# Optimization experiments

Hardware: AMD Instinct MI355X
Metric: run time of the kernel (lower is better)

Reference implementation:

```python
import jax, jax.numpy as jnp
import numpy as np

R = 16       # voxel resolution
CH = 64      # channels
NSAMPLE = 16
PROJ = 3


def _bn(x, p, eps):
    # p: [4, C] rows = (gamma, beta, running_mean, running_var); eval-mode BN
    g, b, m, v = p
    sh = [1] * x.ndim
    sh[1] = -1
    return (x - m.reshape(sh)) * (g.reshape(sh) * jax.lax.rsqrt(v.reshape(sh) + eps)) + b.reshape(sh)


def _gather_ch(x, flat_idx):
    # x: [B, C, M], flat_idx: [B, L] -> [B, C, L]
    B, C, _ = x.shape
    idx = jnp.broadcast_to(flat_idx[:, None, :], (B, C, flat_idx.shape[1]))
    return jnp.take_along_axis(x, idx, axis=2)


def _pvb_forward(x, xyz, idx, w3d1, b3d1, bn3d1, w3d2, b3d2, bn3d2, proj_w1, proj_bn, proj_w2, pt_bn):
    B, C, N = x.shape
    r = R
    # ---------- voxelization (coords detached, normalize=False) ----------
    nc = xyz - xyz.mean(axis=2, keepdims=True)
    nc = jnp.clip((nc + 1.0) * 0.5 * r, 0.0, r - 1.0)
    nc = jax.lax.stop_gradient(nc)                        # [B,3,N] float in [0, r-1]
    vi = jnp.round(nc).astype(jnp.int32)
    flat = (vi[:, 0] * r + vi[:, 1]) * r + vi[:, 2]       # [B,N]
    seg = (flat + jnp.arange(B, dtype=jnp.int32)[:, None] * (r ** 3)).reshape(-1)
    feats = x.transpose(0, 2, 1).reshape(B * N, C)
    sums = jax.ops.segment_sum(feats, seg, num_segments=B * r ** 3)
    cnts = jax.ops.segment_sum(jnp.ones((B * N,), x.dtype), seg, num_segments=B * r ** 3)
    v = (sums / jnp.maximum(cnts, 1.0)[:, None]).reshape(B, r, r, r, C).transpose(0, 4, 1, 2, 3)
    # ---------- depthwise Conv3d -> BN3d -> LeakyReLU (x2) ----------
    dn = ('NCDHW', 'OIDHW', 'NCDHW')
    v = jax.lax.conv_general_dilated(v, w3d1, (1, 1, 1), 'SAME', dimension_numbers=dn,
                                     feature_group_count=C) + b3d1.reshape(1, C, 1, 1, 1)
    v = jax.nn.leaky_relu(_bn(v, bn3d1, 1e-4), 0.1)
    v = jax.lax.conv_general_dilated(v, w3d2, (1, 1, 1), 'SAME', dimension_numbers=dn,
                                     feature_group_count=C) + b3d2.reshape(1, C, 1, 1, 1)
    v = jax.nn.leaky_relu(_bn(v, bn3d2, 1e-4), 0.1)
    # ---------- trilinear devoxelize ----------
    vf = v.reshape(B, C, r ** 3)
    lo = jnp.floor(nc).astype(jnp.int32)
    fr = nc - lo
    hi = jnp.minimum(lo + 1, r - 1)
    p_v_x = jnp.zeros((B, C, N), x.dtype)
    for dx in (0, 1):
        for dy in (0, 1):
            for dz in (0, 1):
                xi = hi[:, 0] if dx else lo[:, 0]
                yi = hi[:, 1] if dy else lo[:, 1]
                zi = hi[:, 2] if dz else lo[:, 2]
                w = ((fr[:, 0] if dx else 1.0 - fr[:, 0]) *
                     (fr[:, 1] if dy else 1.0 - fr[:, 1]) *
                     (fr[:, 2] if dz else 1.0 - fr[:, 2]))
                p_v_x = p_v_x + w[:, None, :] * _gather_ch(vf, (xi * r + yi) * r + zi)
    # ---------- neighbor gather (precomputed ball-query idx) ----------
    K = idx.shape[-1]
    flat_nb = idx.reshape(B, N * K)
    x_j = _gather_ch(x, flat_nb).reshape(B, C, N, K)
    xyz_j = _gather_ch(xyz, flat_nb).reshape(B, 3, N, K)
    dp1 = xyz_j - xyz[:, :, :, None]                      # [B,3,N,K]
    df = x_j - x[:, :, :, None]                           # [B,C,N,K]
    # proj_conv: 1x1 conv -> BN2d -> ReLU -> 1x1 conv
    h = jnp.einsum('oc,bcnk->bonk', proj_w1, df)
    h = jax.nn.relu(_bn(h, proj_bn, 1e-5))
    dp2 = jnp.einsum('oc,bcnk->bonk', proj_w2, h)         # [B,3,N,K]
    dp = jnp.concatenate([dp1, dp2], axis=1)              # [B,6,N,K]
    # repeat_interleave of the 6 channels up to C (last gets remainder)
    part = 6
    rep = C // part
    repeats = np.array([rep] * (part - 1) + [C - rep * (part - 1)])
    w = jnp.repeat(dp, repeats, axis=1, total_repeat_length=C)
    x_j = x_j * w
    x_j = jax.nn.relu(_bn(x_j, pt_bn, 1e-5))              # proj_transform
    p_p_x = x_j.max(axis=-1)                              # max-pool over neighbors
    return p_v_x + p_p_x                                  # agg_way == 'add'


def setup_inputs() -> dict:
    key = jax.random.key(0)
    ks = jax.random.split(key, 16)
    B, C, N, K = 4, CH, 16384, NSAMPLE

    def bn_params(k, c):
        k1, k2, k3, k4 = jax.random.split(k, 4)
        return jnp.stack([1.0 + 0.1 * jax.random.normal(k1, (c,), jnp.float32),
                          0.1 * jax.random.normal(k2, (c,), jnp.float32),
                          0.1 * jax.random.normal(k3, (c,), jnp.float32),
                          jax.random.uniform(k4, (c,), jnp.float32, 0.5, 1.5)])

    return dict(
        x=jax.random.normal(ks[0], (B, C, N), jnp.float32),
        xyz=jax.random.uniform(ks[1], (B, 3, N), jnp.float32, -1.0, 1.0),
        idx=jax.random.randint(ks[2], (B, N, K), 0, N, jnp.int32),
        w3d1=0.1 * jax.random.normal(ks[3], (C, 1, 3, 3, 3), jnp.float32),
        b3d1=0.01 * jax.random.normal(ks[4], (C,), jnp.float32),
        bn3d1=bn_params(ks[5], C),
        w3d2=0.1 * jax.random.normal(ks[6], (C, 1, 3, 3, 3), jnp.float32),
        b3d2=0.01 * jax.random.normal(ks[7], (C,), jnp.float32),
        bn3d2=bn_params(ks[8], C),
        proj_w1=0.1 * jax.random.normal(ks[9], (PROJ, C), jnp.float32),
        proj_bn=bn_params(ks[10], PROJ),
        proj_w2=0.3 * jax.random.normal(ks[11], (PROJ, PROJ), jnp.float32),
        pt_bn=bn_params(ks[12], C),
    )


def reference(x, xyz, idx, w3d1, b3d1, bn3d1, w3d2, b3d2, bn3d2, proj_w1, proj_bn, proj_w2, pt_bn):
    return _pvb_forward(x, xyz, idx, w3d1, b3d1, bn3d1, w3d2, b3d2, bn3d2, proj_w1, proj_bn, proj_w2, pt_bn)
```

## Files before the change

kernel.cpp:

```cpp
#include <hip/hip_runtime.h>

namespace {
constexpr int B_  = 4;
constexpr int C_  = 64;
constexpr int N_  = 16384;
constexpr int K_  = 16;
constexpr int R3_ = 4096;

constexpr int OFF_MEANS = 0;
constexpr int OFF_XT    = 16;
constexpr int OFF_PTS   = OFF_XT   + B_*N_*C_/2;
constexpr int OFF_PTSH  = OFF_PTS  + B_*N_*8;
constexpr int OFF_SUMS  = OFF_PTSH + B_*N_*4;
constexpr int OFF_CNTS  = OFF_SUMS + B_*R3_*C_;
constexpr int OFF_VT16  = OFF_CNTS + B_*R3_;
constexpr int OFF_VOX2  = OFF_VT16 + B_*C_*R3_/2;
constexpr int FILL_FLOATS = B_*R3_*C_ + B_*R3_;
constexpr int FILL_BLOCKS = FILL_FLOATS / (256 * 4);
}

__device__ __forceinline__ unsigned short f2bf(float f) {
  unsigned u = __float_as_uint(f);
  return (unsigned short)((u + 0x7FFFu + ((u >> 16) & 1u)) >> 16);
}
__device__ __forceinline__ unsigned cvtpk_bf16(float lo, float hi) {
  unsigned r;
  asm("v_cvt_pk_bf16_f32 %0, %1, %2" : "=v"(r) : "v"(lo), "v"(hi));
  return r;
}
__device__ __forceinline__ float bflo(unsigned u) { return __uint_as_float(u << 16); }
__device__ __forceinline__ float bfhi(unsigned u) { return __uint_as_float(u & 0xffff0000u); }

__global__ __launch_bounds__(256) void k_init(
    const float* __restrict__ xyz, float* __restrict__ means,
    float* __restrict__ fill) {
  const int blk = blockIdx.x;
  if (blk >= 12) {
    const int base = (blk - 12) * (256 * 4) + threadIdx.x * 4;
    *(float4*)(fill + base) = make_float4(0.f, 0.f, 0.f, 0.f);
    return;
  }
  __shared__ double red[256];
  const float* p = xyz + blk * N_;
  double s = 0.0;
  for (int i = threadIdx.x; i < N_; i += 256) s += (double)p[i];
  red[threadIdx.x] = s;
  __syncthreads();
  for (int st = 128; st; st >>= 1) {
    if (threadIdx.x < st) red[threadIdx.x] += red[threadIdx.x + st];
    __syncthreads();
  }
  if (threadIdx.x == 0) means[blk] = (float)(red[0] * (1.0 / (double)N_));
}

__global__ __launch_bounds__(256) void k_prep(
    const float* __restrict__ x, const float* __restrict__ xyz,
    const float* __restrict__ pw1, const float* __restrict__ means,
    unsigned short* __restrict__ xT, float* __restrict__ pts,
    unsigned* __restrict__ ptsh,
    float* __restrict__ sums, float* __restrict__ cnts) {
  __shared__ float tile[64 * 65];
  __shared__ float ncs[3][64];
  __shared__ float xys[3][64];
  __shared__ float hps[3][64];
  __shared__ int   flats[64];

  const int t   = threadIdx.x;
  const int blk = blockIdx.x;
  const int b   = blk >> 8;
  const int n0  = (blk & 255) << 6;

#pragma unroll
  for (int i = 0; i < 4; ++i) {
    int c = i * 16 + (t >> 4);
    int j4 = (t & 15) * 4;
    float4 v = *(const float4*)&x[((size_t)(b * C_ + c)) * N_ + n0 + j4];
    tile[c * 65 + j4 + 0] = v.x;
    tile[c * 65 + j4 + 1] = v.y;
    tile[c * 65 + j4 + 2] = v.z;
    tile[c * 65 + j4 + 3] = v.w;
  }
  __syncthreads();

  unsigned* __restrict__ xT32 = (unsigned*)xT;
#pragma unroll
  for (int i = 0; i < 8; ++i) {
    int p = i * 8 + (t >> 5);
    int c2 = (t & 31) * 2;
    unsigned pk = cvtpk_bf16(tile[c2 * 65 + p], tile[(c2 + 1) * 65 + p]);
    xT32[((size_t)(b * N_ + n0 + p)) * 32 + (t & 31)] = pk;
  }

  if (t < 192) {
    int p = t & 63, q = t >> 6;
    float s = 0.f;
#pragma unroll
    for (int c = 0; c < 64; ++c) s = fmaf(pw1[q * 64 + c], tile[c * 65 + p], s);
    size_t pb = ((size_t)(b * N_ + n0 + p)) * 8;
    pts[pb + 3 + q] = s;
    hps[q][p] = s;
    float v = xyz[((size_t)(b * 3 + q)) * N_ + n0 + p];
    pts[pb + q] = v;
    xys[q][p] = v;
    float nc = fminf(fmaxf((v - means[b * 3 + q] + 1.0f) * 8.0f, 0.0f), 15.0f);
    ncs[q][p] = nc;
  } else {
    int p = t & 63;
    size_t pb = ((size_t)(b * N_ + n0 + p)) * 8;
    pts[pb + 6] = 0.f;
    pts[pb + 7] = 0.f;
  }
  __syncthreads();

  if (t < 64) {
    int vx = (int)rintf(ncs[0][t]);
    int vy = (int)rintf(ncs[1][t]);
    int vz = (int)rintf(ncs[2][t]);
    int f = (vx * 16 + vy) * 16 + vz;
    flats[t] = f;
    atomicAdd(&cnts[b * R3_ + f], 1.0f);
    uint4 r;
    r.x = cvtpk_bf16(xys[0][t], xys[1][t]);
    r.y = cvtpk_bf16(xys[2][t], hps[0][t]);
    r.z = cvtpk_bf16(hps[1][t], hps[2][t]);
    r.w = 0u;
    *(uint4*)&ptsh[((size_t)(b * N_ + n0 + t)) * 4] = r;
  }
  __syncthreads();

  const int w = t >> 6, lane = t & 63;
#pragma unroll
  for (int i = 0; i < 16; ++i) {
    int p = w * 16 + i;
    int f = flats[p];
    atomicAdd(&sums[((size_t)(b * R3_ + f)) * C_ + lane], tile[lane * 65 + p]);
  }
}

__global__ __launch_bounds__(256) void k_tr(
    const float* __restrict__ sums, const float* __restrict__ cnts,
    unsigned* __restrict__ vT16) {
  __shared__ float tile[64 * 65];
  __shared__ float rs[64];
  const int t = threadIdx.x;
  const int b = blockIdx.x >> 6;
  const int v0 = (blockIdx.x & 63) << 6;

#pragma unroll
  for (int i = 0; i < 16; ++i) {
    int r = i * 4 + (t >> 6);
    int c = t & 63;
    tile[r * 65 + c] = sums[((size_t)(b * R3_ + v0 + r)) * C_ + c];
  }
  if (t < 64) rs[t] = 1.0f / fmaxf(cnts[b * R3_ + v0 + t], 1.0f);
  __syncthreads();

#pragma unroll
  for (int i = 0; i < 8; ++i) {
    int d = t + i * 256;
    int c = d >> 5, vp = (d & 31) * 2;
    unsigned pk = cvtpk_bf16(tile[vp * 65 + c] * rs[vp],
                             tile[(vp + 1) * 65 + c] * rs[vp + 1]);
    vT16[((size_t)(b * C_ + c)) * 2048 + (v0 >> 1) + (d & 31)] = pk;
  }
}

__global__ __launch_bounds__(256) void k_conv(
    const unsigned* __restrict__ vT16,
    const float* __restrict__ w3d1, const float* __restrict__ b3d1,
    const float* __restrict__ bn1, const float* __restrict__ w3d2,
    const float* __restrict__ b3d2, const float* __restrict__ bn2,
    unsigned short* __restrict__ vox2) {
  __shared__ float va[18 * 18 * 20];
  __shared__ float vb[18 * 18 * 20];
  const int t = threadIdx.x;
  const int b = blockIdx.x >> 6;
  const int c = blockIdx.x & 63;

  float W1[27], W2[27];
#pragma unroll
  for (int i = 0; i < 27; ++i) { W1[i] = w3d1[c * 27 + i]; W2[i] = w3d2[c * 27 + i]; }
  const float s1 = bn1[c] / sqrtf(bn1[192 + c] + 1e-4f);
  const float d1 = (b3d1[c] - bn1[128 + c]) * s1 + bn1[64 + c];
  const float s2 = bn2[c] / sqrtf(bn2[192 + c] + 1e-4f);
  const float d2 = (b3d2[c] - bn2[128 + c]) * s2 + bn2[64 + c];

  for (int i = t; i < 18 * 18 * 20; i += 256) { va[i] = 0.f; vb[i] = 0.f; }
  const unsigned* __restrict__ vrow = vT16 + ((size_t)(b * C_ + c)) * 2048;
  __syncthreads();

#pragma unroll
  for (int i = 0; i < 8; ++i) {
    int d = t + i * 256;
    unsigned u = vrow[d];
    int vox0 = d * 2;
    int z = vox0 & 15, y = (vox0 >> 4) & 15, xx = vox0 >> 8;
    int base = ((xx + 1) * 18 + (y + 1)) * 20 + (z + 1);
    va[base]     = bflo(u);
    va[base + 1] = bfhi(u);
  }
  __syncthreads();

  const int x = t >> 4, y = t & 15;
  float acc[16];

#pragma unroll
  for (int z = 0; z < 16; ++z) acc[z] = 0.f;
#pragma unroll
  for (int dx = 0; dx < 3; ++dx)
#pragma unroll
    for (int dy = 0; dy < 3; ++dy) {
      const float* row = &va[((x + dx) * 18 + (y + dy)) * 20];
      float wv[18];
      *(float4*)&wv[0]  = *(const float4*)&row[0];
      *(float4*)&wv[4]  = *(const float4*)&row[4];
      *(float4*)&wv[8]  = *(const float4*)&row[8];
      *(float4*)&wv[12] = *(const float4*)&row[12];
      wv[16] = row[16]; wv[17] = row[17];
      const float k0 = W1[(dx * 3 + dy) * 3 + 0];
      const float k1 = W1[(dx * 3 + dy) * 3 + 1];
      const float k2 = W1[(dx * 3 + dy) * 3 + 2];
#pragma unroll
      for (int z = 0; z < 16; ++z)
        acc[z] = fmaf(k0, wv[z], fmaf(k1, wv[z + 1], fmaf(k2, wv[z + 2], acc[z])));
    }
  {
    const int wb = ((x + 1) * 18 + (y + 1)) * 20 + 1;
#pragma unroll
    for (int z = 0; z < 16; ++z) {
      float tt = acc[z] * s1 + d1;
      vb[wb + z] = tt > 0.f ? tt : 0.1f * tt;
    }
  }
  __syncthreads();

#pragma unroll
  for (int z = 0; z < 16; ++z) acc[z] = 0.f;
#pragma unroll
  for (int dx = 0; dx < 3; ++dx)
#pragma unroll
    for (int dy = 0; dy < 3; ++dy) {
      const float* row = &vb[((x + dx) * 18 + (y + dy)) * 20];
      float wv[18];
      *(float4*)&wv[0]  = *(const float4*)&row[0];
      *(float4*)&wv[4]  = *(const float4*)&row[4];
      *(float4*)&wv[8]  = *(const float4*)&row[8];
      *(float4*)&wv[12] = *(const float4*)&row[12];
      wv[16] = row[16]; wv[17] = row[17];
      const float k0 = W2[(dx * 3 + dy) * 3 + 0];
      const float k1 = W2[(dx * 3 + dy) * 3 + 1];
      const float k2 = W2[(dx * 3 + dy) * 3 + 2];
#pragma unroll
      for (int z = 0; z < 16; ++z)
        acc[z] = fmaf(k0, wv[z], fmaf(k1, wv[z + 1], fmaf(k2, wv[z + 2], acc[z])));
    }
  {
    const int vbase = (x * 16 + y) * 16;
#pragma unroll
    for (int z = 0; z < 16; ++z) {
      float tt = acc[z] * s2 + d2;
      vox2[((size_t)(b * R3_ + vbase + z)) * C_ + c] = f2bf(tt > 0.f ? tt : 0.1f * tt);
    }
  }
}

__global__ __launch_bounds__(256, 8) void k_final(
    const unsigned short* __restrict__ xT, const float* __restrict__ pts,
    const unsigned* __restrict__ ptsh,
    const unsigned short* __restrict__ vox2, const int* __restrict__ idx,
    const float* __restrict__ means, const float* __restrict__ pbn,
    const float* __restrict__ pw2, const float* __restrict__ ptbn,
    float* __restrict__ out) {
  __shared__ unsigned w6[3][513];
  __shared__ int      jarr[512];
  __shared__ unsigned dv[32][8];
  __shared__ float    outT[64 * 33];

  const int t = threadIdx.x;
  const int blk = blockIdx.x;
  const int xcd = blk & 7;
  const int b = xcd >> 1;
  const int t32 = ((blk >> 3) << 1) | (xcd & 1);
  const int n0 = t32 * 32;

  const float psc0 = pbn[0] * rsqrtf(pbn[9]  + 1e-5f);
  const float psc1 = pbn[1] * rsqrtf(pbn[10] + 1e-5f);
  const float psc2 = pbn[2] * rsqrtf(pbn[11] + 1e-5f);
  const float pof0 = pbn[3] - pbn[6] * psc0;
  const float pof1 = pbn[4] - pbn[7] * psc1;
  const float pof2 = pbn[5] - pbn[8] * psc2;
  float W2r[9];
#pragma unroll
  for (int i = 0; i < 9; ++i) W2r[i] = pw2[i];

  const float* __restrict__ ptsb = pts + (size_t)b * N_ * 8;
  const unsigned* __restrict__ ptshb = ptsh + (size_t)b * N_ * 4;

#pragma unroll
  for (int rep = 0; rep < 2; ++rep) {
    const int q = t + rep * 256;
    const int p = q >> 4;
    const int n = n0 + p;
    const int j = idx[(size_t)b * N_ * K_ + (size_t)n0 * K_ + q];
    jarr[q] = j;
    uint4 q4 = *(const uint4*)(ptshb + (size_t)j * 4);
    const float qx0 = bflo(q4.x), qx1 = bfhi(q4.x);
    const float qx2 = bflo(q4.y), qh0 = bfhi(q4.y);
    const float qh1 = bflo(q4.z), qh2 = bfhi(q4.z);
    const float* ir = ptsb + (size_t)n * 8;
    float4 pa = *(const float4*)ir;
    float4 pb = *(const float4*)(ir + 4);
    float d0 = qx0 - pa.x, d1 = qx1 - pa.y, d2 = qx2 - pa.z;
    float c0 = pof0 - psc0 * pa.w;
    float c1 = pof1 - psc1 * pb.x;
    float c2 = pof2 - psc2 * pb.y;
    float h0 = fmaxf(fmaf(qh0, psc0, c0), 0.f);
    float h1 = fmaxf(fmaf(qh1, psc1, c1), 0.f);
    float h2 = fmaxf(fmaf(qh2, psc2, c2), 0.f);
    float e0 = fmaf(W2r[0], h0, fmaf(W2r[1], h1, W2r[2] * h2));
    float e1 = fmaf(W2r[3], h0, fmaf(W2r[4], h1, W2r[5] * h2));
    float e2 = fmaf(W2r[6], h0, fmaf(W2r[7], h1, W2r[8] * h2));
    w6[0][q] = cvtpk_bf16(d0, d1);
    w6[1][q] = cvtpk_bf16(d2, e0);
    w6[2][q] = cvtpk_bf16(e1, e2);
  }

  if (t < 32) {
    const int n = n0 + t;
    const float* ir = ptsb + (size_t)n * 8;
    float x0 = ir[0], x1 = ir[1], x2 = ir[2];
    float nc0 = fminf(fmaxf((x0 - means[b * 3 + 0] + 1.0f) * 8.0f, 0.0f), 15.0f);
    float nc1 = fminf(fmaxf((x1 - means[b * 3 + 1] + 1.0f) * 8.0f, 0.0f), 15.0f);
    float nc2 = fminf(fmaxf((x2 - means[b * 3 + 2] + 1.0f) * 8.0f, 0.0f), 15.0f);
    int lx = (int)nc0, ly = (int)nc1, lz = (int)nc2;
    float fx = nc0 - (float)lx, fy = nc1 - (float)ly, fz = nc2 - (float)lz;
    int hx = lx < 15 ? lx + 1 : 15;
    int hy = ly < 15 ? ly + 1 : 15;
    int hz = lz < 15 ? lz + 1 : 15;
    float wx[2] = {1.f - fx, fx};
    float wy[2] = {1.f - fy, fy};
    float wz[2] = {1.f - fz, fz};
    int xi[2] = {lx, hx}, yi[2] = {ly, hy}, zi[2] = {lz, hz};
#pragma unroll
    for (int c8 = 0; c8 < 8; ++c8) {
      int dx = c8 >> 2, dy = (c8 >> 1) & 1, dz = c8 & 1;
      int flat = (xi[dx] * 16 + yi[dy]) * 16 + zi[dz];
      float wt = wx[dx] * wy[dy] * wz[dz];
      dv[t][c8] = ((unsigned)flat << 16) | (unsigned)f2bf(wt);
    }
  }
  __syncthreads();

  const int w = t >> 6, lane = t & 63;
  const unsigned voff = (unsigned)lane * 2u;
  const int widx = lane < 20 ? 0 : lane < 40 ? 1 : 2;
  const bool hi = (lane >= 10 && lane < 20) || (lane >= 30 && lane < 40) || (lane >= 50);
  const unsigned shl = hi ? 0u : 16u;
  const float ts = ptbn[lane] * rsqrtf(ptbn[192 + lane] + 1e-5f);
  const float td = ptbn[64 + lane] - ptbn[128 + lane] * ts;
  const unsigned short* __restrict__ xTb = xT + (size_t)b * N_ * C_;
  const unsigned short* __restrict__ voxb = vox2 + (size_t)b * R3_ * C_;

  float g[24];
#pragma unroll
  for (int z = 0; z < 24; ++z) g[z] = 0.f;

#pragma unroll
  for (int i = 0; i < 8; ++i) {
    const int p = i * 4 + w;
    const int pq = p * 16;

    unsigned dvu[8];
#pragma unroll
    for (int c8 = 0; c8 < 8; ++c8) {
      dvu[c8] = (unsigned)__builtin_amdgcn_readfirstlane((int)dv[p][c8]);
      const unsigned short* bp = voxb + ((size_t)(dvu[c8] >> 16) << 6);
      asm volatile("global_load_short_d16_hi %0, %1, %2"
                   : "+v"(g[c8]) : "v"(voff), "s"(bp));
    }
#pragma unroll
    for (int k = 0; k < 16; ++k) {
      int jb = __builtin_amdgcn_readfirstlane(jarr[pq + k]);
      const unsigned short* bp = xTb + ((size_t)jb << 6);
      asm volatile("global_load_short_d16_hi %0, %1, %2"
                   : "+v"(g[8 + k]) : "v"(voff), "s"(bp));
    }
    asm volatile("s_waitcnt vmcnt(0)" ::: "memory");
    __builtin_amdgcn_sched_barrier(0);

    float acc = 0.f;
#pragma unroll
    for (int c8 = 0; c8 < 8; ++c8)
      acc = fmaf(__uint_as_float(dvu[c8] << 16), g[c8], acc);

    float pm = 0.f;
#pragma unroll
    for (int k = 0; k < 16; ++k) {
      float wf = __uint_as_float(w6[widx][pq + k] << shl);
      pm = fmaxf(pm, fmaf(g[8 + k] * wf, ts, td));
    }

    outT[lane * 33 + p] = acc + pm;
  }
  __syncthreads();

#pragma unroll
  for (int i = 0; i < 8; ++i) {
    int c = i * 8 + (t >> 5);
    int col = t & 31;
    out[((size_t)(b * C_ + c)) * N_ + n0 + col] = outT[c * 33 + col];
  }
}

extern "C" void kernel_launch(void* const* d_in, const int* in_sizes, int n_in,
                              void* d_out, int out_size, void* d_ws, size_t ws_size,
                              hipStream_t stream) {
  const float* x     = (const float*)d_in[0];
  const float* xyz   = (const float*)d_in[1];
  const int*   idx   = (const int*)  d_in[2];
  const float* w3d1  = (const float*)d_in[3];
  const float* b3d1  = (const float*)d_in[4];
  const float* bn3d1 = (const float*)d_in[5];
  const float* w3d2  = (const float*)d_in[6];
  const float* b3d2  = (const float*)d_in[7];
  const float* bn3d2 = (const float*)d_in[8];
  const float* pw1   = (const float*)d_in[9];
  const float* pbn   = (const float*)d_in[10];
  const float* pw2   = (const float*)d_in[11];
  const float* ptbn  = (const float*)d_in[12];
  float* out = (float*)d_out;
  float* ws  = (float*)d_ws;

  k_init<<<dim3(12 + FILL_BLOCKS), dim3(256), 0, stream>>>(
      xyz, ws + OFF_MEANS, ws + OFF_SUMS);
  k_prep<<<dim3(B_ * N_ / 64), dim3(256), 0, stream>>>(
      x, xyz, pw1, ws + OFF_MEANS, (unsigned short*)(ws + OFF_XT), ws + OFF_PTS,
      (unsigned*)(ws + OFF_PTSH), ws + OFF_SUMS, ws + OFF_CNTS);
  k_tr<<<dim3(B_ * 64), dim3(256), 0, stream>>>(
      ws + OFF_SUMS, ws + OFF_CNTS, (unsigned*)(ws + OFF_VT16));
  k_conv<<<dim3(B_ * C_), dim3(256), 0, stream>>>(
      (const unsigned*)(ws + OFF_VT16), w3d1, b3d1, bn3d1, w3d2, b3d2, bn3d2,
      (unsigned short*)(ws + OFF_VOX2));
  k_final<<<dim3(B_ * N_ / 32), dim3(256), 0, stream>>>(
      (const unsigned short*)(ws + OFF_XT), ws + OFF_PTS,
      (const unsigned*)(ws + OFF_PTSH),
      (const unsigned short*)(ws + OFF_VOX2), idx, ws + OFF_MEANS,
      pbn, pw2, ptbn, out);
}
```

Baseline: 90.66 us.

## Fuse trilinear devoxelization into conv kernel and precompute corner weights in prep

Moves the trilinear devoxelize step out of the final point kernel and into the depthwise conv kernel. Each (batch, channel) block keeps its convolved grid in LDS and gathers from it for all points, instead of writing a bf16 voxel grid to global memory and gathering it per point. Corner indices and weights are now computed once in the prep kernel and stored as a packed per-point table. The cost is a read-modify-write of the full output tensor and a 64x re-read of that table, and the conv kernel now runs only 256 blocks for all the point work.

```diff
diff --git a/kernel.cpp b/kernel.cpp
--- a/kernel.cpp
+++ b/kernel.cpp
@@ -11,10 +11,10 @@
 constexpr int OFF_XT    = 16;
 constexpr int OFF_PTS   = OFF_XT   + B_*N_*C_/2;
 constexpr int OFF_PTSH  = OFF_PTS  + B_*N_*8;
-constexpr int OFF_SUMS  = OFF_PTSH + B_*N_*4;
+constexpr int OFF_DVT   = OFF_PTSH + B_*N_*4;
+constexpr int OFF_SUMS  = OFF_DVT  + B_*N_*8;
 constexpr int OFF_CNTS  = OFF_SUMS + B_*R3_*C_;
 constexpr int OFF_VT16  = OFF_CNTS + B_*R3_;
-constexpr int OFF_VOX2  = OFF_VT16 + B_*C_*R3_/2;
 constexpr int FILL_FLOATS = B_*R3_*C_ + B_*R3_;
 constexpr int FILL_BLOCKS = FILL_FLOATS / (256 * 4);
 }
@@ -22,6 +22,9 @@
 __device__ __forceinline__ unsigned short f2bf(float f) {
   unsigned u = __float_as_uint(f);
   return (unsigned short)((u + 0x7FFFu + ((u >> 16) & 1u)) >> 16);
+}
+__device__ __forceinline__ float bf2f(unsigned short h) {
+  return __uint_as_float(((unsigned)h) << 16);
 }
 __device__ __forceinline__ unsigned cvtpk_bf16(float lo, float hi) {
   unsigned r;
@@ -57,7 +60,7 @@
     const float* __restrict__ x, const float* __restrict__ xyz,
     const float* __restrict__ pw1, const float* __restrict__ means,
     unsigned short* __restrict__ xT, float* __restrict__ pts,
-    unsigned* __restrict__ ptsh,
+    unsigned* __restrict__ ptsh, unsigned* __restrict__ dvt,
     float* __restrict__ sums, float* __restrict__ cnts) {
   __shared__ float tile[64 * 65];
   __shared__ float ncs[3][64];
@@ -113,9 +116,10 @@
   __syncthreads();
 
   if (t < 64) {
-    int vx = (int)rintf(ncs[0][t]);
-    int vy = (int)rintf(ncs[1][t]);
-    int vz = (int)rintf(ncs[2][t]);
+    const float nc0 = ncs[0][t], nc1 = ncs[1][t], nc2 = ncs[2][t];
+    int vx = (int)rintf(nc0);
+    int vy = (int)rintf(nc1);
+    int vz = (int)rintf(nc2);
     int f = (vx * 16 + vy) * 16 + vz;
     flats[t] = f;
     atomicAdd(&cnts[b * R3_ + f], 1.0f);
@@ -125,6 +129,26 @@
     r.z = cvtpk_bf16(hps[1][t], hps[2][t]);
     r.w = 0u;
     *(uint4*)&ptsh[((size_t)(b * N_ + n0 + t)) * 4] = r;
+    int lx = (int)nc0, ly = (int)nc1, lz = (int)nc2;
+    float fx = nc0 - (float)lx, fy = nc1 - (float)ly, fz = nc2 - (float)lz;
+    int hx = lx < 15 ? lx + 1 : 15;
+    int hy = ly < 15 ? ly + 1 : 15;
+    int hz = lz < 15 ? lz + 1 : 15;
+    float wx[2] = {1.f - fx, fx};
+    float wy[2] = {1.f - fy, fy};
+    float wz[2] = {1.f - fz, fz};
+    int xi[2] = {lx, hx}, yi[2] = {ly, hy}, zi[2] = {lz, hz};
+    unsigned c8v[8];
+#pragma unroll
+    for (int c8 = 0; c8 < 8; ++c8) {
+      int dx = c8 >> 2, dy = (c8 >> 1) & 1, dz = c8 & 1;
+      int flat = (xi[dx] * 16 + yi[dy]) * 16 + zi[dz];
+      float wt = wx[dx] * wy[dy] * wz[dz];
+      c8v[c8] = ((unsigned)flat << 16) | (unsigned)f2bf(wt);
+    }
+    unsigned* dp = dvt + ((size_t)(b * N_ + n0 + t)) * 8;
+    *(uint4*)dp       = make_uint4(c8v[0], c8v[1], c8v[2], c8v[3]);
+    *(uint4*)(dp + 4) = make_uint4(c8v[4], c8v[5], c8v[6], c8v[7]);
   }
   __syncthreads();
 
@@ -165,115 +189,13 @@
   }
 }
 
-__global__ __launch_bounds__(256) void k_conv(
-    const unsigned* __restrict__ vT16,
-    const float* __restrict__ w3d1, const float* __restrict__ b3d1,
-    const float* __restrict__ bn1, const float* __restrict__ w3d2,
-    const float* __restrict__ b3d2, const float* __restrict__ bn2,
-    unsigned short* __restrict__ vox2) {
-  __shared__ float va[18 * 18 * 20];
-  __shared__ float vb[18 * 18 * 20];
-  const int t = threadIdx.x;
-  const int b = blockIdx.x >> 6;
-  const int c = blockIdx.x & 63;
-
-  float W1[27], W2[27];
-#pragma unroll
-  for (int i = 0; i < 27; ++i) { W1[i] = w3d1[c * 27 + i]; W2[i] = w3d2[c * 27 + i]; }
-  const float s1 = bn1[c] / sqrtf(bn1[192 + c] + 1e-4f);
-  const float d1 = (b3d1[c] - bn1[128 + c]) * s1 + bn1[64 + c];
-  const float s2 = bn2[c] / sqrtf(bn2[192 + c] + 1e-4f);
-  const float d2 = (b3d2[c] - bn2[128 + c]) * s2 + bn2[64 + c];
-
-  for (int i = t; i < 18 * 18 * 20; i += 256) { va[i] = 0.f; vb[i] = 0.f; }
-  const unsigned* __restrict__ vrow = vT16 + ((size_t)(b * C_ + c)) * 2048;
-  __syncthreads();
-
-#pragma unroll
-  for (int i = 0; i < 8; ++i) {
-    int d = t + i * 256;
-    unsigned u = vrow[d];
-    int vox0 = d * 2;
-    int z = vox0 & 15, y = (vox0 >> 4) & 15, xx = vox0 >> 8;
-    int base = ((xx + 1) * 18 + (y + 1)) * 20 + (z + 1);
-    va[base]     = bflo(u);
-    va[base + 1] = bfhi(u);
-  }
-  __syncthreads();
-
-  const int x = t >> 4, y = t & 15;
-  float acc[16];
-
-#pragma unroll
-  for (int z = 0; z < 16; ++z) acc[z] = 0.f;
-#pragma unroll
-  for (int dx = 0; dx < 3; ++dx)
-#pragma unroll
-    for (int dy = 0; dy < 3; ++dy) {
-      const float* row = &va[((x + dx) * 18 + (y + dy)) * 20];
-      float wv[18];
-      *(float4*)&wv[0]  = *(const float4*)&row[0];
-      *(float4*)&wv[4]  = *(const float4*)&row[4];
-      *(float4*)&wv[8]  = *(const float4*)&row[8];
-      *(float4*)&wv[12] = *(const float4*)&row[12];
-      wv[16] = row[16]; wv[17] = row[17];
-      const float k0 = W1[(dx * 3 + dy) * 3 + 0];
-      const float k1 = W1[(dx * 3 + dy) * 3 + 1];
-      const float k2 = W1[(dx * 3 + dy) * 3 + 2];
-#pragma unroll
-      for (int z = 0; z < 16; ++z)
-        acc[z] = fmaf(k0, wv[z], fmaf(k1, wv[z + 1], fmaf(k2, wv[z + 2], acc[z])));
-    }
-  {
-    const int wb = ((x + 1) * 18 + (y + 1)) * 20 + 1;
-#pragma unroll
-    for (int z = 0; z < 16; ++z) {
-      float tt = acc[z] * s1 + d1;
-      vb[wb + z] = tt > 0.f ? tt : 0.1f * tt;
-    }
-  }
-  __syncthreads();
-
-#pragma unroll
-  for (int z = 0; z < 16; ++z) acc[z] = 0.f;
-#pragma unroll
-  for (int dx = 0; dx < 3; ++dx)
-#pragma unroll
-    for (int dy = 0; dy < 3; ++dy) {
-      const float* row = &vb[((x + dx) * 18 + (y + dy)) * 20];
-      float wv[18];
-      *(float4*)&wv[0]  = *(const float4*)&row[0];
-      *(float4*)&wv[4]  = *(const float4*)&row[4];
-      *(float4*)&wv[8]  = *(const float4*)&row[8];
-      *(float4*)&wv[12] = *(const float4*)&row[12];
-      wv[16] = row[16]; wv[17] = row[17];
-      const float k0 = W2[(dx * 3 + dy) * 3 + 0];
-      const float k1 = W2[(dx * 3 + dy) * 3 + 1];
-      const float k2 = W2[(dx * 3 + dy) * 3 + 2];
-#pragma unroll
-      for (int z = 0; z < 16; ++z)
-        acc[z] = fmaf(k0, wv[z], fmaf(k1, wv[z + 1], fmaf(k2, wv[z + 2], acc[z])));
-    }
-  {
-    const int vbase = (x * 16 + y) * 16;
-#pragma unroll
-    for (int z = 0; z < 16; ++z) {
-      float tt = acc[z] * s2 + d2;
-      vox2[((size_t)(b * R3_ + vbase + z)) * C_ + c] = f2bf(tt > 0.f ? tt : 0.1f * tt);
-    }
-  }
-}
-
-__global__ __launch_bounds__(256, 8) void k_final(
+__global__ __launch_bounds__(256, 8) void k_point(
     const unsigned short* __restrict__ xT, const float* __restrict__ pts,
-    const unsigned* __restrict__ ptsh,
-    const unsigned short* __restrict__ vox2, const int* __restrict__ idx,
-    const float* __restrict__ means, const float* __restrict__ pbn,
-    const float* __restrict__ pw2, const float* __restrict__ ptbn,
-    float* __restrict__ out) {
+    const unsigned* __restrict__ ptsh, const int* __restrict__ idx,
+    const float* __restrict__ pbn, const float* __restrict__ pw2,
+    const float* __restrict__ ptbn, float* __restrict__ out) {
   __shared__ unsigned w6[3][513];
   __shared__ int      jarr[512];
-  __shared__ unsigned dv[32][8];
   __shared__ float    outT[64 * 33];
 
   const int t = threadIdx.x;
@@ -324,83 +246,34 @@
     w6[1][q] = cvtpk_bf16(d2, e0);
     w6[2][q] = cvtpk_bf16(e1, e2);
   }
-
-  if (t < 32) {
-    const int n = n0 + t;
-    const float* ir = ptsb + (size_t)n * 8;
-    float x0 = ir[0], x1 = ir[1], x2 = ir[2];
-    float nc0 = fminf(fmaxf((x0 - means[b * 3 + 0] + 1.0f) * 8.0f, 0.0f), 15.0f);
-    float nc1 = fminf(fmaxf((x1 - means[b * 3 + 1] + 1.0f) * 8.0f, 0.0f), 15.0f);
-    float nc2 = fminf(fmaxf((x2 - means[b * 3 + 2] + 1.0f) * 8.0f, 0.0f), 15.0f);
-    int lx = (int)nc0, ly = (int)nc1, lz = (int)nc2;
-    float fx = nc0 - (float)lx, fy = nc1 - (float)ly, fz = nc2 - (float)lz;
-    int hx = lx < 15 ? lx + 1 : 15;
-    int hy = ly < 15 ? ly + 1 : 15;
-    int hz = lz < 15 ? lz + 1 : 15;
-    float wx[2] = {1.f - fx, fx};
-    float wy[2] = {1.f - fy, fy};
-    float wz[2] = {1.f - fz, fz};
-    int xi[2] = {lx, hx}, yi[2] = {ly, hy}, zi[2] = {lz, hz};
-#pragma unroll
-    for (int c8 = 0; c8 < 8; ++c8) {
-      int dx = c8 >> 2, dy = (c8 >> 1) & 1, dz = c8 & 1;
-      int flat = (xi[dx] * 16 + yi[dy]) * 16 + zi[dz];
-      float wt = wx[dx] * wy[dy] * wz[dz];
-      dv[t][c8] = ((unsigned)flat << 16) | (unsigned)f2bf(wt);
-    }
-  }
   __syncthreads();
 
   const int w = t >> 6, lane = t & 63;
-  const unsigned voff = (unsigned)lane * 2u;
   const int widx = lane < 20 ? 0 : lane < 40 ? 1 : 2;
   const bool hi = (lane >= 10 && lane < 20) || (lane >= 30 && lane < 40) || (lane >= 50);
   const unsigned shl = hi ? 0u : 16u;
   const float ts = ptbn[lane] * rsqrtf(ptbn[192 + lane] + 1e-5f);
   const float td = ptbn[64 + lane] - ptbn[128 + lane] * ts;
   const unsigned short* __restrict__ xTb = xT + (size_t)b * N_ * C_;
-  const unsigned short* __restrict__ voxb = vox2 + (size_t)b * R3_ * C_;
-
-  float g[24];
-#pragma unroll
-  for (int z = 0; z < 24; ++z) g[z] = 0.f;
 
 #pragma unroll
   for (int i = 0; i < 8; ++i) {
     const int p = i * 4 + w;
     const int pq = p * 16;
 
-    unsigned dvu[8];
-#pragma unroll
-    for (int c8 = 0; c8 < 8; ++c8) {
-      dvu[c8] = (unsigned)__builtin_amdgcn_readfirstlane((int)dv[p][c8]);
-      const unsigned short* bp = voxb + ((size_t)(dvu[c8] >> 16) << 6);
-      asm volatile("global_load_short_d16_hi %0, %1, %2"
-                   : "+v"(g[c8]) : "v"(voff), "s"(bp));
-    }
-#pragma unroll
-    for (int k = 0; k < 16; ++k) {
-      int jb = __builtin_amdgcn_readfirstlane(jarr[pq + k]);
-      const unsigned short* bp = xTb + ((size_t)jb << 6);
-      asm volatile("global_load_short_d16_hi %0, %1, %2"
-                   : "+v"(g[8 + k]) : "v"(voff), "s"(bp));
-    }
-    asm volatile("s_waitcnt vmcnt(0)" ::: "memory");
-    __builtin_amdgcn_sched_barrier(0);
-
-    float acc = 0.f;
-#pragma unroll
-    for (int c8 = 0; c8 < 8; ++c8)
-      acc = fmaf(__uint_as_float(dvu[c8] << 16), g[c8], acc);
+    unsigned short xjv[16];
+#pragma unroll
+    for (int k = 0; k < 16; ++k)
+      xjv[k] = xTb[(size_t)jarr[pq + k] * C_ + lane];
 
     float pm = 0.f;
 #pragma unroll
     for (int k = 0; k < 16; ++k) {
       float wf = __uint_as_float(w6[widx][pq + k] << shl);
-      pm = fmaxf(pm, fmaf(g[8 + k] * wf, ts, td));
-    }
-
-    outT[lane * 33 + p] = acc + pm;
+      pm = fmaxf(pm, fmaf(bf2f(xjv[k]) * wf, ts, td));
+    }
+
+    outT[lane * 33 + p] = pm;
   }
   __syncthreads();
 
@@ -409,6 +282,127 @@
     int c = i * 8 + (t >> 5);
     int col = t & 31;
     out[((size_t)(b * C_ + c)) * N_ + n0 + col] = outT[c * 33 + col];
+  }
+}
+
+__global__ __launch_bounds__(256) void k_convdevox(
+    const unsigned* __restrict__ vT16,
+    const float* __restrict__ w3d1, const float* __restrict__ b3d1,
+    const float* __restrict__ bn1, const float* __restrict__ w3d2,
+    const float* __restrict__ b3d2, const float* __restrict__ bn2,
+    const unsigned* __restrict__ dvt, float* __restrict__ out) {
+  __shared__ float va[18 * 18 * 20];
+  __shared__ float vb[18 * 18 * 20];
+  __shared__ float vls[R3_];
+  const int t = threadIdx.x;
+  const int b = blockIdx.x >> 6;
+  const int c = blockIdx.x & 63;
+
+  float W1[27], W2[27];
+#pragma unroll
+  for (int i = 0; i < 27; ++i) { W1[i] = w3d1[c * 27 + i]; W2[i] = w3d2[c * 27 + i]; }
+  const float s1 = bn1[c] / sqrtf(bn1[192 + c] + 1e-4f);
+  const float d1 = (b3d1[c] - bn1[128 + c]) * s1 + bn1[64 + c];
+  const float s2 = bn2[c] / sqrtf(bn2[192 + c] + 1e-4f);
+  const float d2 = (b3d2[c] - bn2[128 + c]) * s2 + bn2[64 + c];
+
+  for (int i = t; i < 18 * 18 * 20; i += 256) { va[i] = 0.f; vb[i] = 0.f; }
+  const unsigned* __restrict__ vrow = vT16 + ((size_t)(b * C_ + c)) * 2048;
+  __syncthreads();
+
+#pragma unroll
+  for (int i = 0; i < 8; ++i) {
+    int d = t + i * 256;
+    unsigned u = vrow[d];
+    int vox0 = d * 2;
+    int z = vox0 & 15, y = (vox0 >> 4) & 15, xx = vox0 >> 8;
+    int base = ((xx + 1) * 18 + (y + 1)) * 20 + (z + 1);
+    va[base]     = bflo(u);
+    va[base + 1] = bfhi(u);
+  }
+  __syncthreads();
+
+  const int x = t >> 4, y = t & 15;
+  float acc[16];
+
+#pragma unroll
+  for (int z = 0; z < 16; ++z) acc[z] = 0.f;
+#pragma unroll
+  for (int dx = 0; dx < 3; ++dx)
+#pragma unroll
+    for (int dy = 0; dy < 3; ++dy) {
+      const float* row = &va[((x + dx) * 18 + (y + dy)) * 20];
+      float wv[18];
+      *(float4*)&wv[0]  = *(const float4*)&row[0];
+      *(float4*)&wv[4]  = *(const float4*)&row[4];
+      *(float4*)&wv[8]  = *(const float4*)&row[8];
+      *(float4*)&wv[12] = *(const float4*)&row[12];
+      wv[16] = row[16]; wv[17] = row[17];
+      const float k0 = W1[(dx * 3 + dy) * 3 + 0];
+      const float k1 = W1[(dx * 3 + dy) * 3 + 1];
+      const float k2 = W1[(dx * 3 + dy) * 3 + 2];
+#pragma unroll
+      for (int z = 0; z < 16; ++z)
+        acc[z] = fmaf(k0, wv[z], fmaf(k1, wv[z + 1], fmaf(k2, wv[z + 2], acc[z])));
+    }
+  {
+    const int wb = ((x + 1) * 18 + (y + 1)) * 20 + 1;
+#pragma unroll
+    for (int z = 0; z < 16; ++z) {
+      float tt = acc[z] * s1 + d1;
+      vb[wb + z] = tt > 0.f ? tt : 0.1f * tt;
+    }
+  }
+  __syncthreads();
+
+#pragma unroll
+  for (int z = 0; z < 16; ++z) acc[z] = 0.f;
+#pragma unroll
+  for (int dx = 0; dx < 3; ++dx)
+#pragma unroll
+    for (int dy = 0; dy < 3; ++dy) {
+      const float* row = &vb[((x + dx) * 18 + (y + dy)) * 20];
+      float wv[18];
+      *(float4*)&wv[0]  = *(const float4*)&row[0];
+      *(float4*)&wv[4]  = *(const float4*)&row[4];
+      *(float4*)&wv[8]  = *(const float4*)&row[8];
+      *(float4*)&wv[12] = *(const float4*)&row[12];
+      wv[16] = row[16]; wv[17] = row[17];
+      const float k0 = W2[(dx * 3 + dy) * 3 + 0];
+      const float k1 = W2[(dx * 3 + dy) * 3 + 1];
+      const float k2 = W2[(dx * 3 + dy) * 3 + 2];
+#pragma unroll
+      for (int z = 0; z < 16; ++z)
+        acc[z] = fmaf(k0, wv[z], fmaf(k1, wv[z + 1], fmaf(k2, wv[z + 2], acc[z])));
+    }
+  {
+    const int vbase = (x * 16 + y) * 16;
+#pragma unroll
+    for (int z = 0; z < 16; ++z) {
+      float tt = acc[z] * s2 + d2;
+      vls[vbase + z] = tt > 0.f ? tt : 0.1f * tt;
+    }
+  }
+  __syncthreads();
+
+  const uint4* __restrict__ dv4 = (const uint4*)(dvt + (size_t)b * N_ * 8);
+  float* __restrict__ orow = out + ((size_t)(b * C_ + c)) * N_;
+#pragma unroll 4
+  for (int i = 0; i < 64; ++i) {
+    const int n = t + i * 256;
+    uint4 a = dv4[n * 2];
+    uint4 bq = dv4[n * 2 + 1];
+    float o = orow[n];
+    float dacc;
+    dacc = bflo(a.x)  * vls[a.x  >> 16];
+    dacc = fmaf(bflo(a.y),  vls[a.y  >> 16], dacc);
+    dacc = fmaf(bflo(a.z),  vls[a.z  >> 16], dacc);
+    dacc = fmaf(bflo(a.w),  vls[a.w  >> 16], dacc);
+    dacc = fmaf(bflo(bq.x), vls[bq.x >> 16], dacc);
+    dacc = fmaf(bflo(bq.y), vls[bq.y >> 16], dacc);
+    dacc = fmaf(bflo(bq.z), vls[bq.z >> 16], dacc);
+    dacc = fmaf(bflo(bq.w), vls[bq.w >> 16], dacc);
+    orow[n] = o + dacc;
   }
 }
 
@@ -435,15 +429,14 @@
       xyz, ws + OFF_MEANS, ws + OFF_SUMS);
   k_prep<<<dim3(B_ * N_ / 64), dim3(256), 0, stream>>>(
       x, xyz, pw1, ws + OFF_MEANS, (unsigned short*)(ws + OFF_XT), ws + OFF_PTS,
-      (unsigned*)(ws + OFF_PTSH), ws + OFF_SUMS, ws + OFF_CNTS);
+      (unsigned*)(ws + OFF_PTSH), (unsigned*)(ws + OFF_DVT),
+      ws + OFF_SUMS, ws + OFF_CNTS);
   k_tr<<<dim3(B_ * 64), dim3(256), 0, stream>>>(
       ws + OFF_SUMS, ws + OFF_CNTS, (unsigned*)(ws + OFF_VT16));
-  k_conv<<<dim3(B_ * C_), dim3(256), 0, stream>>>(
+  k_point<<<dim3(B_ * N_ / 32), dim3(256), 0, stream>>>(
+      (const unsigned short*)(ws + OFF_XT), ws + OFF_PTS,
+      (const unsigned*)(ws + OFF_PTSH), idx, pbn, pw2, ptbn, out);
+  k_convdevox<<<dim3(B_ * C_), dim3(256), 0, stream>>>(
       (const unsigned*)(ws + OFF_VT16), w3d1, b3d1, bn3d1, w3d2, b3d2, bn3d2,
-      (unsigned short*)(ws + OFF_VOX2));
-  k_final<<<dim3(B_ * N_ / 32), dim3(256), 0, stream>>>(
-      (const unsigned short*)(ws + OFF_XT), ws + OFF_PTS,
-      (const unsigned*)(ws + OFF_PTSH),
-      (const unsigned short*)(ws + OFF_VOX2), idx, ws + OFF_MEANS,
-      pbn, pw2, ptbn, out);
-}
+      (const unsigned*)(ws + OFF_DVT), out);
+}
```

After: 90.88 us. No clear change (+0.2%).
